# Performance work log

Measured on AMD Instinct MI355X. Metric: run time of the kernel, lower is better.

Reference implementation:

```python
import jax, jax.numpy as jnp
import numpy as np

FILTER_SIZES = [3, 5, 7, 11, 15, 23, 37, 55]
NB_GROUP = 8
CHAN = 512
IN_CHAN = 3


def setup_inputs() -> dict:
    key = jax.random.key(0)
    keys = jax.random.split(key, 2 + 2 * len(FILTER_SIZES))
    B, H, W = 2, 128, 128
    cpf = CHAN // len(FILTER_SIZES)  # 64 channels per filter size
    inp = {"x": jax.random.normal(keys[0], (B, IN_CHAN, H, W), jnp.float32)}
    for i, k in enumerate(FILTER_SIZES):
        fan_in = IN_CHAN * k * k
        inp[f"w{i}"] = jax.random.normal(keys[1 + 2 * i], (cpf, IN_CHAN, k, k), jnp.float32) / np.sqrt(fan_in).astype(np.float32)
        inp[f"b{i}"] = 0.01 * jax.random.normal(keys[2 + 2 * i], (cpf,), jnp.float32)
    # torch.randperm channel shuffle, fixed for determinism
    inp["perm"] = jax.random.permutation(keys[-1], CHAN)
    return inp


def _conv_relu(x, w, b, k):
    p = (k - 1) // 2  # same padding (odd filter sizes)
    y = jax.lax.conv_general_dilated(
        x, w, window_strides=(1, 1), padding=[(p, p), (p, p)],
        dimension_numbers=("NCHW", "OIHW", "NCHW"))
    return jax.nn.relu(y + b[None, :, None, None])


def reference(x, w0, b0, w1, b1, w2, b2, w3, b3, w4, b4, w5, b5, w6, b6, w7, b7, perm):
    ws = [w0, w1, w2, w3, w4, w5, w6, w7]
    bs = [b0, b1, b2, b3, b4, b5, b6, b7]
    feats = [_conv_relu(x, ws[i], bs[i], FILTER_SIZES[i]) for i in range(len(FILTER_SIZES))]
    feat = jnp.concatenate(feats, axis=1)          # [B, 512, H, W]
    feat = feat[:, perm]                            # channel shuffle
    B, C, H, W = feat.shape
    g = NB_GROUP
    s = C // g
    # unfold(1,s,s)+permute(0,1,4,2,3) == reshape to [B, g, s, H, W]
    feat = feat.reshape(B * g, s, H * W)            # [B*g, s, HW]
    # graham order 2: (feat[:, :, None] * feat[:, None, :]).sum(-1) as a contraction
    gram = jnp.einsum("bcn,bdn->bcd", feat, feat)  # [B*g, s, s]
    return gram.reshape(B, g, s * s)                # [B, g, s*s]
```

## Files before the change

kernel.cpp:

```cpp
#include <hip/hip_runtime.h>
#include <hip/hip_bf16.h>
#include <cstdint>

typedef __attribute__((ext_vector_type(8))) short short8;
typedef __attribute__((ext_vector_type(4))) short short4v;
typedef __attribute__((ext_vector_type(4))) float f32x4;

static constexpr int HWPIX = 16384;
static constexpr int NCH   = 512;
static constexpr int GCHK  = 32;

__device__ __forceinline__ unsigned short f2bf(float f) {
    unsigned int u = __float_as_uint(f);
    u = (u + 0x7fffu + ((u >> 16) & 1u)) >> 16;
    return (unsigned short)u;
}

template<int K> struct KG {
    static constexpr int P     = (K - 1) / 2;
    static constexpr int NSEC  = (K + 7) / 8;
    static constexpr int SEGS  = 3 * K;
    static constexpr int NCHK  = (SEGS + 3) / 4;
    static constexpr int NCHKP = ((NCHK + 3) / 4) * 4;
    static constexpr int COLS  = 64 + K - 1;
    static constexpr int XPAD  = 128;
    static constexpr int XSE   = COLS * 24 + XPAD;
};
static_assert(1512 + KG< 3>::NCHKP * 32 <= KG< 3>::XSE, "pad3");
static_assert(1512 + KG< 5>::NCHKP * 32 <= KG< 5>::XSE, "pad5");
static_assert(1512 + KG< 7>::NCHKP * 32 <= KG< 7>::XSE, "pad7");
static_assert(1512 + KG<11>::NCHKP * 32 <= KG<11>::XSE, "pad11");
static_assert(1512 + KG<15>::NCHKP * 32 <= KG<15>::XSE, "pad15");
static_assert(1512 + KG<23>::NCHKP * 32 <= KG<23>::XSE, "pad23");
static_assert(1512 + KG<37>::NCHKP * 32 <= KG<37>::XSE, "pad37");
static_assert(1512 + KG<55>::NCHKP * 32 <= KG<55>::XSE, "pad55");
static_assert(KG<55>::XSE * 2 <= 18432, "xs fits smem");

struct PtrArgs {
    const float* w[8];
    const float* bias[8];
    unsigned short* wpk[8];
    int cum[9];
};

template<int K>
__device__ void repack_body(const float* __restrict__ w, unsigned short* __restrict__ wpk, int t) {
    constexpr int NCHKP = KG<K>::NCHKP;
    const int sec = t / NCHKP;
    const int tc  = t - sec * NCHKP;
    const int tid = threadIdx.x;
    const int co  = ((tid >> 6) << 4) + (tid & 15);
    const int seg = tc * 4 + ((tid >> 4) & 3);
    int kw = 0, r = 0;
    const bool vseg = seg < KG<K>::SEGS;
    if (vseg) { kw = seg / 3; r = seg - kw * 3; }
    short8 o;
    #pragma unroll
    for (int j = 0; j < 8; ++j) {
        const int icr = r * 8 + j;
        const int ic  = icr >> 3;
        const int kh  = sec * 8 + (icr & 7);
        float v = 0.f;
        if (vseg && kh < K)
            v = w[((co * 3 + ic) * K + kh) * K + kw];
        o[j] = (short)f2bf(v);
    }
    *reinterpret_cast<short8*>(wpk + ((size_t)(t * 256 + tid)) * 8) = o;
}

__global__ __launch_bounds__(256) void repack_all(PtrArgs a) {
    const int blk = blockIdx.x;
    int f = 0;
    #pragma unroll
    for (int i = 0; i < 8; ++i) if (blk >= a.cum[i + 1]) f = i + 1;
    const int t = blk - a.cum[f];
    switch (f) {
        case 0: repack_body< 3>(a.w[0], a.wpk[0], t); break;
        case 1: repack_body< 5>(a.w[1], a.wpk[1], t); break;
        case 2: repack_body< 7>(a.w[2], a.wpk[2], t); break;
        case 3: repack_body<11>(a.w[3], a.wpk[3], t); break;
        case 4: repack_body<15>(a.w[4], a.wpk[4], t); break;
        case 5: repack_body<23>(a.w[5], a.wpk[5], t); break;
        case 6: repack_body<37>(a.w[6], a.wpk[6], t); break;
        case 7: repack_body<55>(a.w[7], a.wpk[7], t); break;
    }
}

#define MFMA_BF16 __builtin_amdgcn_mfma_f32_16x16x32_bf16

template<int K>
__device__ void conv_body(const float* __restrict__ x, const unsigned short* __restrict__ wpk,
                          const float* __restrict__ bias, unsigned short* __restrict__ feat,
                          int cbase, char* smem, int bx)
{
    constexpr int P     = KG<K>::P;
    constexpr int NCHKP = KG<K>::NCHKP;
    constexpr int NSEC  = KG<K>::NSEC;
    constexpr int COLS  = KG<K>::COLS;

    unsigned short* xs = (unsigned short*)smem;
    float* red = (float*)smem;

    const int tid = threadIdx.x;
    const int ph  = bx & 1;
    const int h   = (bx >> 1) & 127;
    const int b   = bx >> 8;

    const int lane = tid & 63;
    const int wv   = tid >> 6;
    const int ln15 = lane & 15;
    const int lg   = lane >> 4;

    for (int i = tid * 4; i < KG<K>::XPAD; i += 1024)
        *reinterpret_cast<short4v*>(xs + COLS * 24 + i) = short4v{0, 0, 0, 0};

    f32x4 acc[4][4] = {};
    const float* xb = x + (size_t)b * 3 * HWPIX;
    const int col0 = ph * 64 - P;

    for (int sec = 0; sec < NSEC; ++sec) {
        if (sec > 0) __syncthreads();
        for (int e = tid * 4; e < 24 * COLS; e += 1024) {
            const int c  = e / 24;
            const int i0 = e - c * 24;
            const int col = col0 + c;
            short4v pk;
            #pragma unroll
            for (int j = 0; j < 4; ++j) {
                const int icr = i0 + j;
                const int ic  = icr >> 3;
                const int row = h + sec * 8 + (icr & 7) - P;
                float v = 0.f;
                if ((unsigned)row < 128u && (unsigned)col < 128u)
                    v = xb[ic * HWPIX + row * 128 + col];
                pk[j] = (short)f2bf(v);
            }
            *reinterpret_cast<short4v*>(xs + e) = pk;
        }
        __syncthreads();

        const unsigned short* ws = wpk + (size_t)sec * NCHKP * 2048 + lane * 8;
        for (int tt = 0; tt < NCHKP / 4; ++tt) {
            const int t = tt * 4 + wv;
            const unsigned short* ap = ws + (size_t)t * 2048;
            short8 a0 = *reinterpret_cast<const short8*>(ap);
            short8 a1 = *reinterpret_cast<const short8*>(ap + 512);
            short8 a2 = *reinterpret_cast<const short8*>(ap + 1024);
            short8 a3 = *reinterpret_cast<const short8*>(ap + 1536);
            const unsigned short* bp = xs + ln15 * 24 + lg * 8 + t * 32;
            short8 b0 = *reinterpret_cast<const short8*>(bp);
            short8 b1 = *reinterpret_cast<const short8*>(bp + 1 * 384);
            short8 b2 = *reinterpret_cast<const short8*>(bp + 2 * 384);
            short8 b3 = *reinterpret_cast<const short8*>(bp + 3 * 384);

            acc[0][0] = MFMA_BF16(a0, b0, acc[0][0], 0, 0, 0);
            acc[0][1] = MFMA_BF16(a0, b1, acc[0][1], 0, 0, 0);
            acc[0][2] = MFMA_BF16(a0, b2, acc[0][2], 0, 0, 0);
            acc[0][3] = MFMA_BF16(a0, b3, acc[0][3], 0, 0, 0);
            acc[1][0] = MFMA_BF16(a1, b0, acc[1][0], 0, 0, 0);
            acc[1][1] = MFMA_BF16(a1, b1, acc[1][1], 0, 0, 0);
            acc[1][2] = MFMA_BF16(a1, b2, acc[1][2], 0, 0, 0);
            acc[1][3] = MFMA_BF16(a1, b3, acc[1][3], 0, 0, 0);
            acc[2][0] = MFMA_BF16(a2, b0, acc[2][0], 0, 0, 0);
            acc[2][1] = MFMA_BF16(a2, b1, acc[2][1], 0, 0, 0);
            acc[2][2] = MFMA_BF16(a2, b2, acc[2][2], 0, 0, 0);
            acc[2][3] = MFMA_BF16(a2, b3, acc[2][3], 0, 0, 0);
            acc[3][0] = MFMA_BF16(a3, b0, acc[3][0], 0, 0, 0);
            acc[3][1] = MFMA_BF16(a3, b1, acc[3][1], 0, 0, 0);
            acc[3][2] = MFMA_BF16(a3, b2, acc[3][2], 0, 0, 0);
            acc[3][3] = MFMA_BF16(a3, b3, acc[3][3], 0, 0, 0);
        }
    }

    __syncthreads();
    const float bv  = bias[tid >> 2];
    const int   eco = tid >> 2;
    const int   ep0 = (tid & 3) * 4;
    const size_t fbase = (((size_t)(b * NCH + cbase + eco)) << 14) + h * 128 + ph * 64;

    #pragma unroll
    for (int q = 0; q < 4; ++q) {
        if (q > 0) __syncthreads();
        #pragma unroll
        for (int cs = 0; cs < 4; ++cs)
            #pragma unroll
            for (int i = 0; i < 4; ++i)
                red[(wv * 64 + cs * 16 + lg * 4 + i) * 18 + ln15] = acc[cs][q][i];
        __syncthreads();
        short4v o;
        #pragma unroll
        for (int j = 0; j < 4; ++j) {
            const int px = ep0 + j;
            float v = red[(0 * 64 + eco) * 18 + px] + red[(1 * 64 + eco) * 18 + px]
                    + red[(2 * 64 + eco) * 18 + px] + red[(3 * 64 + eco) * 18 + px];
            o[j] = (short)f2bf(fmaxf(v + bv, 0.f));
        }
        *reinterpret_cast<short4v*>(feat + fbase + q * 16 + ep0) = o;
    }
}

__global__ __launch_bounds__(256, 3) void conv_all(const float* __restrict__ x,
                                                   PtrArgs a, unsigned short* __restrict__ feat)
{
    __shared__ __align__(16) char smem[18432];
    switch (7 - blockIdx.y) {
        case 0: conv_body< 3>(x, a.wpk[0], a.bias[0], feat, 0 * 64, smem, blockIdx.x); break;
        case 1: conv_body< 5>(x, a.wpk[1], a.bias[1], feat, 1 * 64, smem, blockIdx.x); break;
        case 2: conv_body< 7>(x, a.wpk[2], a.bias[2], feat, 2 * 64, smem, blockIdx.x); break;
        case 3: conv_body<11>(x, a.wpk[3], a.bias[3], feat, 3 * 64, smem, blockIdx.x); break;
        case 4: conv_body<15>(x, a.wpk[4], a.bias[4], feat, 4 * 64, smem, blockIdx.x); break;
        case 5: conv_body<23>(x, a.wpk[5], a.bias[5], feat, 5 * 64, smem, blockIdx.x); break;
        case 6: conv_body<37>(x, a.wpk[6], a.bias[6], feat, 6 * 64, smem, blockIdx.x); break;
        case 7: conv_body<55>(x, a.wpk[7], a.bias[7], feat, 7 * 64, smem, blockIdx.x); break;
    }
}

__global__ __launch_bounds__(256) void gram_mfma(
    const unsigned short* __restrict__ feat, const int* __restrict__ perm,
    float* __restrict__ part)
{
    __shared__ __align__(16) unsigned short tile[64 * 256];
    __shared__ int permch[64];

    const int bg = blockIdx.y, chunk = blockIdx.x;
    const int b = bg >> 3, gq = bg & 7;
    const int tid = threadIdx.x;

    if (tid < 64) permch[tid] = perm[gq * 64 + tid];
    __syncthreads();

    const int lane = tid & 63;
    const int wv   = tid >> 6;
    const int ln15 = lane & 15;
    const int kg   = lane >> 4;

    f32x4 acc[4] = {};
    const size_t pxbase = (size_t)chunk * 512;

    for (int p2 = 0; p2 < 2; ++p2) {
        {
            const int r0 = tid >> 5;
            const int g  = tid & 31;
            #pragma unroll
            for (int it = 0; it < 8; ++it) {
                const int r = it * 8 + r0;
                const unsigned short* src =
                    feat + (((size_t)(b * NCH + permch[r])) << 14) + pxbase + p2 * 256 + g * 8;
                short8 v = *reinterpret_cast<const short8*>(src);
                *reinterpret_cast<short8*>(tile + r * 256 + ((g ^ (r & 7)) * 8)) = v;
            }
        }
        __syncthreads();
        #pragma unroll
        for (int t = 0; t < 8; ++t) {
            const int g  = t * 4 + kg;
            const int ra = wv * 16 + ln15;
            short8 av = *reinterpret_cast<const short8*>(tile + ra * 256 + ((g ^ (ra & 7)) * 8));
            #pragma unroll
            for (int cs = 0; cs < 4; ++cs) {
                const int rb = cs * 16 + ln15;
                short8 bv = *reinterpret_cast<const short8*>(tile + rb * 256 + ((g ^ (rb & 7)) * 8));
                acc[cs] = MFMA_BF16(av, bv, acc[cs], 0, 0, 0);
            }
        }
        __syncthreads();
    }

    float* pp = part + ((size_t)bg * GCHK + chunk) * 4096;
    #pragma unroll
    for (int cs = 0; cs < 4; ++cs)
        #pragma unroll
        for (int i = 0; i < 4; ++i) {
            const int row = wv * 16 + kg * 4 + i;
            const int col = cs * 16 + ln15;
            pp[row * 64 + col] = acc[cs][i];
        }
}

__global__ __launch_bounds__(256) void gram_reduce(
    const float* __restrict__ part, float* __restrict__ out)
{
    const int idx = blockIdx.x * 256 + threadIdx.x;
    const int bg  = idx >> 12;
    const int e   = idx & 4095;
    const float* p = part + (size_t)bg * GCHK * 4096 + e;
    float s = 0.f;
    #pragma unroll
    for (int c = 0; c < GCHK; ++c) s += p[c * 4096];
    out[idx] = s;
}

extern "C" void kernel_launch(void* const* d_in, const int* in_sizes, int n_in,
                              void* d_out, int out_size, void* d_ws, size_t ws_size,
                              hipStream_t stream) {
    const float* x = (const float*)d_in[0];
    const int* perm = (const int*)d_in[17];

    unsigned short* feat = (unsigned short*)d_ws;
    float* part = (float*)((char*)d_ws + (size_t)2 * NCH * HWPIX * sizeof(unsigned short));
    unsigned short* wpk0 = (unsigned short*)((char*)part + (size_t)16 * GCHK * 4096 * sizeof(float));
    float* out = (float*)d_out;

    const int nchk[8] = { KG<3>::NSEC * KG<3>::NCHKP,  KG<5>::NSEC * KG<5>::NCHKP,
                          KG<7>::NSEC * KG<7>::NCHKP,  KG<11>::NSEC * KG<11>::NCHKP,
                          KG<15>::NSEC * KG<15>::NCHKP, KG<23>::NSEC * KG<23>::NCHKP,
                          KG<37>::NSEC * KG<37>::NCHKP, KG<55>::NSEC * KG<55>::NCHKP };
    PtrArgs a;
    int acc = 0;
    for (int i = 0; i < 8; ++i) {
        a.w[i]    = (const float*)d_in[1 + 2 * i];
        a.bias[i] = (const float*)d_in[2 + 2 * i];
        a.wpk[i]  = wpk0 + (size_t)acc * 2048;
        a.cum[i]  = acc;
        acc += nchk[i];
    }
    a.cum[8] = acc;

    repack_all<<<acc, 256, 0, stream>>>(a);
    conv_all<<<dim3(512, 8), 256, 0, stream>>>(x, a, feat);
    gram_mfma<<<dim3(GCHK, 16), 256, 0, stream>>>(feat, perm, part);
    gram_reduce<<<dim3(65536 / 256), 256, 0, stream>>>(part, out);
}
```

Before: 111.9 us.

## Use 32x32x16 MFMA with full-row conv tiles and double-buffered input staging

The conv kernel now has each block cover a full 128-pixel output row instead of half a row, and switches from 16x16x32 to 32x32x16 bf16 MFMA. Weights are repacked for 32-channel strips with 16-deep K chunks. Input staging is double-buffered in shared memory, so the next kernel-row section is loaded while the current one is being multiplied. This is meant to improve MFMA efficiency, cut redundant halo loads, and overlap staging with compute. The cost is twice the shared memory, a lower occupancy bound (2 blocks/SM instead of 3), and half as many blocks in the grid.

```diff
diff --git a/kernel.cpp b/kernel.cpp
--- a/kernel.cpp
+++ b/kernel.cpp
@@ -5,6 +5,7 @@
 typedef __attribute__((ext_vector_type(8))) short short8;
 typedef __attribute__((ext_vector_type(4))) short short4v;
 typedef __attribute__((ext_vector_type(4))) float f32x4;
+typedef __attribute__((ext_vector_type(16))) float f32x16;
 
 static constexpr int HWPIX = 16384;
 static constexpr int NCH   = 512;
@@ -17,24 +18,24 @@
 }
 
 template<int K> struct KG {
-    static constexpr int P     = (K - 1) / 2;
-    static constexpr int NSEC  = (K + 7) / 8;
-    static constexpr int SEGS  = 3 * K;
-    static constexpr int NCHK  = (SEGS + 3) / 4;
-    static constexpr int NCHKP = ((NCHK + 3) / 4) * 4;
-    static constexpr int COLS  = 64 + K - 1;
-    static constexpr int XPAD  = 128;
-    static constexpr int XSE   = COLS * 24 + XPAD;
+    static constexpr int P       = (K - 1) / 2;
+    static constexpr int NSEC    = (K + 7) / 8;
+    static constexpr int SEGS    = 3 * K;
+    static constexpr int NCHK16  = (SEGS + 1) / 2;
+    static constexpr int NCHKP16 = ((NCHK16 + 3) / 4) * 4;
+    static constexpr int COLS    = 128 + K - 1;
+    static constexpr int XPAD    = 128;
+    static constexpr int XSE     = COLS * 24 + XPAD;
 };
-static_assert(1512 + KG< 3>::NCHKP * 32 <= KG< 3>::XSE, "pad3");
-static_assert(1512 + KG< 5>::NCHKP * 32 <= KG< 5>::XSE, "pad5");
-static_assert(1512 + KG< 7>::NCHKP * 32 <= KG< 7>::XSE, "pad7");
-static_assert(1512 + KG<11>::NCHKP * 32 <= KG<11>::XSE, "pad11");
-static_assert(1512 + KG<15>::NCHKP * 32 <= KG<15>::XSE, "pad15");
-static_assert(1512 + KG<23>::NCHKP * 32 <= KG<23>::XSE, "pad23");
-static_assert(1512 + KG<37>::NCHKP * 32 <= KG<37>::XSE, "pad37");
-static_assert(1512 + KG<55>::NCHKP * 32 <= KG<55>::XSE, "pad55");
-static_assert(KG<55>::XSE * 2 <= 18432, "xs fits smem");
+static_assert(3048 + KG< 3>::NCHKP16 * 16 <= KG< 3>::XSE, "pad3");
+static_assert(3048 + KG< 5>::NCHKP16 * 16 <= KG< 5>::XSE, "pad5");
+static_assert(3048 + KG< 7>::NCHKP16 * 16 <= KG< 7>::XSE, "pad7");
+static_assert(3048 + KG<11>::NCHKP16 * 16 <= KG<11>::XSE, "pad11");
+static_assert(3048 + KG<15>::NCHKP16 * 16 <= KG<15>::XSE, "pad15");
+static_assert(3048 + KG<23>::NCHKP16 * 16 <= KG<23>::XSE, "pad23");
+static_assert(3048 + KG<37>::NCHKP16 * 16 <= KG<37>::XSE, "pad37");
+static_assert(3048 + KG<55>::NCHKP16 * 16 <= KG<55>::XSE, "pad55");
+static_assert(2 * KG<55>::XSE * 2 <= 33792, "dbuf fits smem");
 
 struct PtrArgs {
     const float* w[8];
@@ -45,12 +46,15 @@
 
 template<int K>
 __device__ void repack_body(const float* __restrict__ w, unsigned short* __restrict__ wpk, int t) {
-    constexpr int NCHKP = KG<K>::NCHKP;
-    const int sec = t / NCHKP;
-    const int tc  = t - sec * NCHKP;
+    constexpr int NCHKP16 = KG<K>::NCHKP16;
+    const int sec = t / NCHKP16;
+    const int t16 = t - sec * NCHKP16;
     const int tid = threadIdx.x;
-    const int co  = ((tid >> 6) << 4) + (tid & 15);
-    const int seg = tc * 4 + ((tid >> 4) & 3);
+    if (tid >= 128) return;
+    const int strip = tid >> 6;
+    const int lane  = tid & 63;
+    const int co    = strip * 32 + (lane & 31);
+    const int seg   = 2 * t16 + (lane >> 5);
     int kw = 0, r = 0;
     const bool vseg = seg < KG<K>::SEGS;
     if (vseg) { kw = seg / 3; r = seg - kw * 3; }
@@ -65,7 +69,7 @@
             v = w[((co * 3 + ic) * K + kh) * K + kw];
         o[j] = (short)f2bf(v);
     }
-    *reinterpret_cast<short8*>(wpk + ((size_t)(t * 256 + tid)) * 8) = o;
+    *reinterpret_cast<short8*>(wpk + ((size_t)t * 128 + strip * 64 + lane) * 8) = o;
 }
 
 __global__ __launch_bounds__(256) void repack_all(PtrArgs a) {
@@ -86,44 +90,43 @@
     }
 }
 
-#define MFMA_BF16 __builtin_amdgcn_mfma_f32_16x16x32_bf16
+#define MFMA32 __builtin_amdgcn_mfma_f32_32x32x16_bf16
 
 template<int K>
 __device__ void conv_body(const float* __restrict__ x, const unsigned short* __restrict__ wpk,
                           const float* __restrict__ bias, unsigned short* __restrict__ feat,
                           int cbase, char* smem, int bx)
 {
-    constexpr int P     = KG<K>::P;
-    constexpr int NCHKP = KG<K>::NCHKP;
-    constexpr int NSEC  = KG<K>::NSEC;
-    constexpr int COLS  = KG<K>::COLS;
-
-    unsigned short* xs = (unsigned short*)smem;
+    constexpr int P        = KG<K>::P;
+    constexpr int NCHKP16  = KG<K>::NCHKP16;
+    constexpr int NSEC     = KG<K>::NSEC;
+    constexpr int COLS     = KG<K>::COLS;
+    constexpr int XSE      = KG<K>::XSE;
+
+    unsigned short* xs0 = (unsigned short*)smem;
     float* red = (float*)smem;
 
     const int tid = threadIdx.x;
-    const int ph  = bx & 1;
-    const int h   = (bx >> 1) & 127;
-    const int b   = bx >> 8;
+    const int b   = bx >> 7;
+    const int h   = bx & 127;
 
     const int lane = tid & 63;
     const int wv   = tid >> 6;
-    const int ln15 = lane & 15;
-    const int lg   = lane >> 4;
-
-    for (int i = tid * 4; i < KG<K>::XPAD; i += 1024)
-        *reinterpret_cast<short4v*>(xs + COLS * 24 + i) = short4v{0, 0, 0, 0};
-
-    f32x4 acc[4][4] = {};
+    const int l31  = lane & 31;
+    const int lh   = lane >> 5;
+
     const float* xb = x + (size_t)b * 3 * HWPIX;
-    const int col0 = ph * 64 - P;
-
-    for (int sec = 0; sec < NSEC; ++sec) {
-        if (sec > 0) __syncthreads();
+
+    for (int i = tid * 4; i < KG<K>::XPAD; i += 1024) {
+        *reinterpret_cast<short4v*>(xs0 + COLS * 24 + i)       = short4v{0, 0, 0, 0};
+        *reinterpret_cast<short4v*>(xs0 + XSE + COLS * 24 + i) = short4v{0, 0, 0, 0};
+    }
+
+    auto stage = [&](int sec, unsigned short* dst) {
         for (int e = tid * 4; e < 24 * COLS; e += 1024) {
             const int c  = e / 24;
             const int i0 = e - c * 24;
-            const int col = col0 + c;
+            const int col = c - P;
             short4v pk;
             #pragma unroll
             for (int j = 0; j < 4; ++j) {
@@ -135,74 +138,76 @@
                     v = xb[ic * HWPIX + row * 128 + col];
                 pk[j] = (short)f2bf(v);
             }
-            *reinterpret_cast<short4v*>(xs + e) = pk;
-        }
-        __syncthreads();
-
-        const unsigned short* ws = wpk + (size_t)sec * NCHKP * 2048 + lane * 8;
-        for (int tt = 0; tt < NCHKP / 4; ++tt) {
-            const int t = tt * 4 + wv;
-            const unsigned short* ap = ws + (size_t)t * 2048;
+            *reinterpret_cast<short4v*>(dst + e) = pk;
+        }
+    };
+
+    stage(0, xs0);
+    __syncthreads();
+
+    f32x16 acc[2][4] = {};
+
+    for (int s = 0; s < NSEC; ++s) {
+        if (s + 1 < NSEC) stage(s + 1, xs0 + ((s + 1) & 1) * XSE);
+
+        const unsigned short* xsR  = xs0 + (s & 1) * XSE;
+        const unsigned short* wsec = wpk + (size_t)s * NCHKP16 * 1024 + lane * 8;
+
+        for (int tt = 0; tt < NCHKP16 / 4; ++tt) {
+            const int t16 = tt * 4 + wv;
+            const unsigned short* ap = wsec + (size_t)t16 * 1024;
             short8 a0 = *reinterpret_cast<const short8*>(ap);
             short8 a1 = *reinterpret_cast<const short8*>(ap + 512);
-            short8 a2 = *reinterpret_cast<const short8*>(ap + 1024);
-            short8 a3 = *reinterpret_cast<const short8*>(ap + 1536);
-            const unsigned short* bp = xs + ln15 * 24 + lg * 8 + t * 32;
+            const unsigned short* bp = xsR + l31 * 24 + lh * 8 + t16 * 16;
             short8 b0 = *reinterpret_cast<const short8*>(bp);
-            short8 b1 = *reinterpret_cast<const short8*>(bp + 1 * 384);
-            short8 b2 = *reinterpret_cast<const short8*>(bp + 2 * 384);
-            short8 b3 = *reinterpret_cast<const short8*>(bp + 3 * 384);
-
-            acc[0][0] = MFMA_BF16(a0, b0, acc[0][0], 0, 0, 0);
-            acc[0][1] = MFMA_BF16(a0, b1, acc[0][1], 0, 0, 0);
-            acc[0][2] = MFMA_BF16(a0, b2, acc[0][2], 0, 0, 0);
-            acc[0][3] = MFMA_BF16(a0, b3, acc[0][3], 0, 0, 0);
-            acc[1][0] = MFMA_BF16(a1, b0, acc[1][0], 0, 0, 0);
-            acc[1][1] = MFMA_BF16(a1, b1, acc[1][1], 0, 0, 0);
-            acc[1][2] = MFMA_BF16(a1, b2, acc[1][2], 0, 0, 0);
-            acc[1][3] = MFMA_BF16(a1, b3, acc[1][3], 0, 0, 0);
-            acc[2][0] = MFMA_BF16(a2, b0, acc[2][0], 0, 0, 0);
-            acc[2][1] = MFMA_BF16(a2, b1, acc[2][1], 0, 0, 0);
-            acc[2][2] = MFMA_BF16(a2, b2, acc[2][2], 0, 0, 0);
-            acc[2][3] = MFMA_BF16(a2, b3, acc[2][3], 0, 0, 0);
-            acc[3][0] = MFMA_BF16(a3, b0, acc[3][0], 0, 0, 0);
-            acc[3][1] = MFMA_BF16(a3, b1, acc[3][1], 0, 0, 0);
-            acc[3][2] = MFMA_BF16(a3, b2, acc[3][2], 0, 0, 0);
-            acc[3][3] = MFMA_BF16(a3, b3, acc[3][3], 0, 0, 0);
-        }
-    }
-
-    __syncthreads();
+            short8 b1 = *reinterpret_cast<const short8*>(bp + 768);
+            short8 b2 = *reinterpret_cast<const short8*>(bp + 1536);
+            short8 b3 = *reinterpret_cast<const short8*>(bp + 2304);
+
+            acc[0][0] = MFMA32(a0, b0, acc[0][0], 0, 0, 0);
+            acc[0][1] = MFMA32(a0, b1, acc[0][1], 0, 0, 0);
+            acc[0][2] = MFMA32(a0, b2, acc[0][2], 0, 0, 0);
+            acc[0][3] = MFMA32(a0, b3, acc[0][3], 0, 0, 0);
+            acc[1][0] = MFMA32(a1, b0, acc[1][0], 0, 0, 0);
+            acc[1][1] = MFMA32(a1, b1, acc[1][1], 0, 0, 0);
+            acc[1][2] = MFMA32(a1, b2, acc[1][2], 0, 0, 0);
+            acc[1][3] = MFMA32(a1, b3, acc[1][3], 0, 0, 0);
+        }
+        __syncthreads();
+    }
+
     const float bv  = bias[tid >> 2];
     const int   eco = tid >> 2;
-    const int   ep0 = (tid & 3) * 4;
-    const size_t fbase = (((size_t)(b * NCH + cbase + eco)) << 14) + h * 128 + ph * 64;
+    const int   px8 = (tid & 3) * 8;
+    const size_t fbase = (((size_t)(b * NCH + cbase + eco)) << 14) + h * 128;
 
     #pragma unroll
     for (int q = 0; q < 4; ++q) {
         if (q > 0) __syncthreads();
         #pragma unroll
-        for (int cs = 0; cs < 4; ++cs)
+        for (int strip = 0; strip < 2; ++strip)
             #pragma unroll
-            for (int i = 0; i < 4; ++i)
-                red[(wv * 64 + cs * 16 + lg * 4 + i) * 18 + ln15] = acc[cs][q][i];
+            for (int reg = 0; reg < 16; ++reg) {
+                const int co = strip * 32 + (reg & 3) + 8 * (reg >> 2) + 4 * lh;
+                red[(wv * 64 + co) * 33 + l31] = acc[strip][q][reg];
+            }
         __syncthreads();
-        short4v o;
+        short8 o;
         #pragma unroll
-        for (int j = 0; j < 4; ++j) {
-            const int px = ep0 + j;
-            float v = red[(0 * 64 + eco) * 18 + px] + red[(1 * 64 + eco) * 18 + px]
-                    + red[(2 * 64 + eco) * 18 + px] + red[(3 * 64 + eco) * 18 + px];
+        for (int j = 0; j < 8; ++j) {
+            const int px = px8 + j;
+            float v = red[(0 * 64 + eco) * 33 + px] + red[(1 * 64 + eco) * 33 + px]
+                    + red[(2 * 64 + eco) * 33 + px] + red[(3 * 64 + eco) * 33 + px];
             o[j] = (short)f2bf(fmaxf(v + bv, 0.f));
         }
-        *reinterpret_cast<short4v*>(feat + fbase + q * 16 + ep0) = o;
-    }
-}
-
-__global__ __launch_bounds__(256, 3) void conv_all(const float* __restrict__ x,
+        *reinterpret_cast<short8*>(feat + fbase + q * 32 + px8) = o;
+    }
+}
+
+__global__ __launch_bounds__(256, 2) void conv_all(const float* __restrict__ x,
                                                    PtrArgs a, unsigned short* __restrict__ feat)
 {
-    __shared__ __align__(16) char smem[18432];
+    __shared__ __align__(16) char smem[33792];
     switch (7 - blockIdx.y) {
         case 0: conv_body< 3>(x, a.wpk[0], a.bias[0], feat, 0 * 64, smem, blockIdx.x); break;
         case 1: conv_body< 5>(x, a.wpk[1], a.bias[1], feat, 1 * 64, smem, blockIdx.x); break;
@@ -214,6 +219,8 @@
         case 7: conv_body<55>(x, a.wpk[7], a.bias[7], feat, 7 * 64, smem, blockIdx.x); break;
     }
 }
+
+#define MFMA_BF16 __builtin_amdgcn_mfma_f32_16x16x32_bf16
 
 __global__ __launch_bounds__(256) void gram_mfma(
     const unsigned short* __restrict__ feat, const int* __restrict__ perm,
@@ -301,23 +308,23 @@
     unsigned short* wpk0 = (unsigned short*)((char*)part + (size_t)16 * GCHK * 4096 * sizeof(float));
     float* out = (float*)d_out;
 
-    const int nchk[8] = { KG<3>::NSEC * KG<3>::NCHKP,  KG<5>::NSEC * KG<5>::NCHKP,
-                          KG<7>::NSEC * KG<7>::NCHKP,  KG<11>::NSEC * KG<11>::NCHKP,
-                          KG<15>::NSEC * KG<15>::NCHKP, KG<23>::NSEC * KG<23>::NCHKP,
-                          KG<37>::NSEC * KG<37>::NCHKP, KG<55>::NSEC * KG<55>::NCHKP };
+    const int nchk[8] = { KG<3>::NSEC * KG<3>::NCHKP16,  KG<5>::NSEC * KG<5>::NCHKP16,
+                          KG<7>::NSEC * KG<7>::NCHKP16,  KG<11>::NSEC * KG<11>::NCHKP16,
+                          KG<15>::NSEC * KG<15>::NCHKP16, KG<23>::NSEC * KG<23>::NCHKP16,
+                          KG<37>::NSEC * KG<37>::NCHKP16, KG<55>::NSEC * KG<55>::NCHKP16 };
     PtrArgs a;
     int acc = 0;
     for (int i = 0; i < 8; ++i) {
         a.w[i]    = (const float*)d_in[1 + 2 * i];
         a.bias[i] = (const float*)d_in[2 + 2 * i];
-        a.wpk[i]  = wpk0 + (size_t)acc * 2048;
+        a.wpk[i]  = wpk0 + (size_t)acc * 1024;
         a.cum[i]  = acc;
         acc += nchk[i];
     }
     a.cum[8] = acc;
 
     repack_all<<<acc, 256, 0, stream>>>(a);
-    conv_all<<<dim3(512, 8), 256, 0, stream>>>(x, a, feat);
+    conv_all<<<dim3(256, 8), 256, 0, stream>>>(x, a, feat);
     gram_mfma<<<dim3(GCHK, 16), 256, 0, stream>>>(feat, perm, part);
     gram_reduce<<<dim3(65536 / 256), 256, 0, stream>>>(part, out);
 }
```

Result: faster. 105.8 us (-5.4%).

## Process full 128-pixel row per conv block, split waves across K and pixel halves

Applied to the files above, without the earlier changes.

Each conv block now covers a whole 128-column output row instead of a 64-column half. The four waves are split into two K-chunk groups and two pixel halves, which halves the cross-wave reduction fan-in and halves the grid. The aim is to reuse each staged input row and each loaded weight fragment across twice as many pixels and to amortize the halo columns. The trade-off is half as many blocks, which means less parallelism, twice as many MFMA K-iterations per wave, and a larger shared-memory input tile.

```diff
diff --git a/kernel.cpp b/kernel.cpp
--- a/kernel.cpp
+++ b/kernel.cpp
@@ -22,19 +22,14 @@
     static constexpr int SEGS  = 3 * K;
     static constexpr int NCHK  = (SEGS + 3) / 4;
     static constexpr int NCHKP = ((NCHK + 3) / 4) * 4;
-    static constexpr int COLS  = 64 + K - 1;
+    static constexpr int COLS  = 128 + K - 1;
     static constexpr int XPAD  = 128;
     static constexpr int XSE   = COLS * 24 + XPAD;
 };
-static_assert(1512 + KG< 3>::NCHKP * 32 <= KG< 3>::XSE, "pad3");
-static_assert(1512 + KG< 5>::NCHKP * 32 <= KG< 5>::XSE, "pad5");
-static_assert(1512 + KG< 7>::NCHKP * 32 <= KG< 7>::XSE, "pad7");
-static_assert(1512 + KG<11>::NCHKP * 32 <= KG<11>::XSE, "pad11");
-static_assert(1512 + KG<15>::NCHKP * 32 <= KG<15>::XSE, "pad15");
-static_assert(1512 + KG<23>::NCHKP * 32 <= KG<23>::XSE, "pad23");
-static_assert(1512 + KG<37>::NCHKP * 32 <= KG<37>::XSE, "pad37");
-static_assert(1512 + KG<55>::NCHKP * 32 <= KG<55>::XSE, "pad55");
+static_assert(127 * 24 + (KG<55>::NCHKP * 4 - 1) * 8 + 8 <= KG<55>::XSE, "pad55");
+static_assert(127 * 24 + (KG<11>::NCHKP * 4 - 1) * 8 + 8 <= KG<11>::XSE, "pad11");
 static_assert(KG<55>::XSE * 2 <= 18432, "xs fits smem");
+static_assert(2 * 2 * 64 * 18 * 4 <= 18432, "red fits smem");
 
 struct PtrArgs {
     const float* w[8];
@@ -102,12 +97,13 @@
     float* red = (float*)smem;
 
     const int tid = threadIdx.x;
-    const int ph  = bx & 1;
-    const int h   = (bx >> 1) & 127;
-    const int b   = bx >> 8;
+    const int b   = bx >> 7;
+    const int h   = bx & 127;
 
     const int lane = tid & 63;
     const int wv   = tid >> 6;
+    const int kq   = wv >> 1;
+    const int pq   = wv & 1;
     const int ln15 = lane & 15;
     const int lg   = lane >> 4;
 
@@ -116,14 +112,13 @@
 
     f32x4 acc[4][4] = {};
     const float* xb = x + (size_t)b * 3 * HWPIX;
-    const int col0 = ph * 64 - P;
 
     for (int sec = 0; sec < NSEC; ++sec) {
         if (sec > 0) __syncthreads();
         for (int e = tid * 4; e < 24 * COLS; e += 1024) {
             const int c  = e / 24;
             const int i0 = e - c * 24;
-            const int col = col0 + c;
+            const int col = c - P;
             short4v pk;
             #pragma unroll
             for (int j = 0; j < 4; ++j) {
@@ -140,14 +135,14 @@
         __syncthreads();
 
         const unsigned short* ws = wpk + (size_t)sec * NCHKP * 2048 + lane * 8;
-        for (int tt = 0; tt < NCHKP / 4; ++tt) {
-            const int t = tt * 4 + wv;
+        for (int tt = 0; tt < NCHKP / 2; ++tt) {
+            const int t = tt * 2 + kq;
             const unsigned short* ap = ws + (size_t)t * 2048;
             short8 a0 = *reinterpret_cast<const short8*>(ap);
             short8 a1 = *reinterpret_cast<const short8*>(ap + 512);
             short8 a2 = *reinterpret_cast<const short8*>(ap + 1024);
             short8 a3 = *reinterpret_cast<const short8*>(ap + 1536);
-            const unsigned short* bp = xs + ln15 * 24 + lg * 8 + t * 32;
+            const unsigned short* bp = xs + (pq * 64 + ln15) * 24 + lg * 8 + t * 32;
             short8 b0 = *reinterpret_cast<const short8*>(bp);
             short8 b1 = *reinterpret_cast<const short8*>(bp + 1 * 384);
             short8 b2 = *reinterpret_cast<const short8*>(bp + 2 * 384);
@@ -176,7 +171,7 @@
     const float bv  = bias[tid >> 2];
     const int   eco = tid >> 2;
     const int   ep0 = (tid & 3) * 4;
-    const size_t fbase = (((size_t)(b * NCH + cbase + eco)) << 14) + h * 128 + ph * 64;
+    const size_t fbase = (((size_t)(b * NCH + cbase + eco)) << 14) + h * 128;
 
     #pragma unroll
     for (int q = 0; q < 4; ++q) {
@@ -185,17 +180,20 @@
         for (int cs = 0; cs < 4; ++cs)
             #pragma unroll
             for (int i = 0; i < 4; ++i)
-                red[(wv * 64 + cs * 16 + lg * 4 + i) * 18 + ln15] = acc[cs][q][i];
+                red[pq * 2304 + (kq * 64 + cs * 16 + lg * 4 + i) * 18 + ln15] = acc[cs][q][i];
         __syncthreads();
-        short4v o;
         #pragma unroll
-        for (int j = 0; j < 4; ++j) {
-            const int px = ep0 + j;
-            float v = red[(0 * 64 + eco) * 18 + px] + red[(1 * 64 + eco) * 18 + px]
-                    + red[(2 * 64 + eco) * 18 + px] + red[(3 * 64 + eco) * 18 + px];
-            o[j] = (short)f2bf(fmaxf(v + bv, 0.f));
-        }
-        *reinterpret_cast<short4v*>(feat + fbase + q * 16 + ep0) = o;
+        for (int half = 0; half < 2; ++half) {
+            short4v o;
+            #pragma unroll
+            for (int j = 0; j < 4; ++j) {
+                const int px = ep0 + j;
+                float v = red[half * 2304 + eco * 18 + px]
+                        + red[half * 2304 + (64 + eco) * 18 + px];
+                o[j] = (short)f2bf(fmaxf(v + bv, 0.f));
+            }
+            *reinterpret_cast<short4v*>(feat + fbase + half * 64 + q * 16 + ep0) = o;
+        }
     }
 }
 
@@ -317,7 +315,7 @@
     a.cum[8] = acc;
 
     repack_all<<<acc, 256, 0, stream>>>(a);
-    conv_all<<<dim3(512, 8), 256, 0, stream>>>(x, a, feat);
+    conv_all<<<dim3(256, 8), 256, 0, stream>>>(x, a, feat);
     gram_mfma<<<dim3(GCHK, 16), 256, 0, stream>>>(feat, perm, part);
     gram_reduce<<<dim3(65536 / 256), 256, 0, stream>>>(part, out);
 }
```

Measured after the change: 118.8 us. 1.06x slower.
